# Kernel optimization log

Measured on AMD Instinct MI355X. Metric: run time of the kernel, lower is better.

## Reference

```python
import jax, jax.numpy as jnp
import numpy as np

HEADS = 4
DIM_HEAD = 32
SCALE = 16.0
EPS = 1e-5  # jax.nn.standardize default


def _standardize(t):
    # standardize over last axis (the flattened x*y*z sequence), per (b, h, d)
    mu = jnp.mean(t, axis=-1, keepdims=True)
    var = jnp.var(t, axis=-1, keepdims=True)
    return (t - mu) * jax.lax.rsqrt(var + EPS)


def setup_inputs() -> dict:
    key = jax.random.key(0)
    k1, k2, k3 = jax.random.split(key, 3)
    dim = 64
    hidden = HEADS * DIM_HEAD  # 128
    b, x, y, z = 2, 16, 16, 16
    inp = jax.random.normal(k1, (b, x, y, z, dim), dtype=jnp.float32)
    # 1x1x1 convs == pointwise channel matmuls; init like flax lecun_normal-ish scale
    w_qkv = jax.random.normal(k2, (dim, 3 * hidden), dtype=jnp.float32) / np.sqrt(dim)
    w_out = jax.random.normal(k3, (hidden, dim), dtype=jnp.float32) / np.sqrt(hidden)
    b_out = jnp.zeros((dim,), dtype=jnp.float32)
    return {"input": inp, "w_qkv": w_qkv, "w_out": w_out, "b_out": b_out}


def reference(input, w_qkv, w_out, b_out):
    b, x, y, z, c = input.shape
    s = x * y * z
    # pointwise conv -> qkv
    qkv = jnp.einsum('bxyzc,cd->bxyzd', input, w_qkv)  # [b,x,y,z,3*hidden]
    q, k, v = jnp.split(qkv, 3, axis=-1)
    # rearrange 'b x y z (h c) -> b h c (x y z)'
    def to_bhds(t):
        return t.reshape(b, s, HEADS, DIM_HEAD).transpose(0, 2, 3, 1)  # [b,h,d,s]
    q, k, v = map(to_bhds, (q, k, v))
    q = _standardize(q)
    k = _standardize(k)
    sim = jnp.einsum('bhdi,bhdj->bhij', q, k) * SCALE  # [b,h,s,s]
    attn = jax.nn.softmax(sim, axis=-1)
    out = jnp.einsum('bhij,bhdj->bhid', attn, v)  # [b,h,s,d]
    # rearrange 'b h (x y z) d -> b x y z (h d)'
    out = out.transpose(0, 2, 1, 3).reshape(b, x, y, z, HEADS * DIM_HEAD)
    return jnp.einsum('bxyzc,co->bxyzo', out, w_out) + b_out
```

## Files before the change

### kernel.cpp

```cpp
#include <hip/hip_runtime.h>
#include <math.h>
#include <stdint.h>


typedef __attribute__((ext_vector_type(8))) short short8;
typedef __attribute__((ext_vector_type(4))) float f32x4;
typedef __attribute__((ext_vector_type(16))) float f32x16;

#define QSCALE 23.083120654223414f

#if __has_builtin(__builtin_amdgcn_exp2f)
#define EXP2F(x) __builtin_amdgcn_exp2f(x)
#else
#define EXP2F(x) exp2f(x)
#endif

__device__ inline uint32_t pack_hilo(float y) {
  uint32_t uy = __float_as_uint(y);
  uint32_t hb = (uy + 0x7fffu + ((uy >> 16) & 1u)) >> 16;
  float hf = __uint_as_float(hb << 16);
  float r = y - hf;
  uint32_t ur = __float_as_uint(r);
  uint32_t lb = (ur + 0x7fffu + ((ur >> 16) & 1u)) >> 16;
  return (hb << 16) | (lb & 0xffffu);
}

__device__ inline ushort f32_to_bf16(float y) {
  uint32_t uy = __float_as_uint(y);
  return (ushort)((uy + 0x7fffu + ((uy >> 16) & 1u)) >> 16);
}

__device__ inline float bpermf(int addr, float v) {
  return __int_as_float(__builtin_amdgcn_ds_bpermute(addr, __float_as_int(v)));
}

__device__ inline short8 as_s8(uint4 v) {
  union { uint4 u; short8 s; } t;
  t.u = v;
  return t.s;
}

__global__ __launch_bounds__(256) void qkv_kernel(const float* __restrict__ in,
                                                  const float* __restrict__ w,
                                                  float* __restrict__ qf,
                                                  float* __restrict__ kf,
                                                  ushort* __restrict__ vfr,
                                                  float* __restrict__ psum,
                                                  float* __restrict__ psq) {
  __shared__ char smem[18432];
  __shared__ float ssum[64], ssq[64];
  ushort* Bh = (ushort*)smem;
  ushort* Bl = (ushort*)(smem + 9216);
  float* VT = (float*)smem;

  const int ctile = blockIdx.x % 6;
  const int stile = blockIdx.x / 6;
  const int tid = threadIdx.x;
  const int row0 = stile * 64;
  const int sel = ctile >> 1;

  if (tid < 64) { ssum[tid] = 0.f; ssq[tid] = 0.f; }

  {
    const int col = tid & 63;
    const int k0 = (tid >> 6) * 16;
    const float* wp = w + (size_t)k0 * 384 + ctile * 64 + col;
    float xv[16];
#pragma unroll
    for (int j = 0; j < 16; ++j) xv[j] = wp[(size_t)j * 384];
    uint32_t hi[8], lo[8];
#pragma unroll
    for (int p = 0; p < 8; ++p) {
      const uint32_t u0 = __float_as_uint(xv[2 * p]);
      const uint32_t u1 = __float_as_uint(xv[2 * p + 1]);
      hi[p] = __builtin_amdgcn_perm(u1, u0, 0x07060302u);
      const float d0 = xv[2 * p] - __uint_as_float(u0 & 0xffff0000u);
      const float d1 = xv[2 * p + 1] - __uint_as_float(u1 & 0xffff0000u);
      lo[p] = __builtin_amdgcn_perm(__float_as_uint(d1), __float_as_uint(d0), 0x07060302u);
    }
    uint4* bh = (uint4*)&Bh[col * 72 + k0];
    bh[0] = make_uint4(hi[0], hi[1], hi[2], hi[3]);
    bh[1] = make_uint4(hi[4], hi[5], hi[6], hi[7]);
    uint4* bl = (uint4*)&Bl[col * 72 + k0];
    bl[0] = make_uint4(lo[0], lo[1], lo[2], lo[3]);
    bl[1] = make_uint4(lo[4], lo[5], lo[6], lo[7]);
  }
  __syncthreads();

  const int wv = tid >> 6, lane = tid & 63;
  const int wr = wv >> 1, wc = wv & 1;
  const int h2 = lane >> 5, pl = lane & 31;

  short8 ah[4], al[4];
  {
    const float* ap = in + (size_t)(row0 + wr * 32 + pl) * 64 + h2 * 8;
#pragma unroll
    for (int kb = 0; kb < 4; ++kb) {
      const float4 xa = *(const float4*)(ap + kb * 16);
      const float4 xb = *(const float4*)(ap + kb * 16 + 4);
      const float xs[8] = {xa.x, xa.y, xa.z, xa.w, xb.x, xb.y, xb.z, xb.w};
      uint32_t hp[4], lp[4];
#pragma unroll
      for (int p = 0; p < 4; ++p) {
        const uint32_t u0 = __float_as_uint(xs[2 * p]);
        const uint32_t u1 = __float_as_uint(xs[2 * p + 1]);
        hp[p] = __builtin_amdgcn_perm(u1, u0, 0x07060302u);
        const float d0 = xs[2 * p] - __uint_as_float(u0 & 0xffff0000u);
        const float d1 = xs[2 * p + 1] - __uint_as_float(u1 & 0xffff0000u);
        lp[p] = __builtin_amdgcn_perm(__float_as_uint(d1), __float_as_uint(d0), 0x07060302u);
      }
      union { uint32_t u[4]; short8 s; } th, tl;
      th.u[0] = hp[0]; th.u[1] = hp[1]; th.u[2] = hp[2]; th.u[3] = hp[3];
      tl.u[0] = lp[0]; tl.u[1] = lp[1]; tl.u[2] = lp[2]; tl.u[3] = lp[3];
      ah[kb] = th.s;
      al[kb] = tl.s;
    }
  }

  const ushort* bhp = &Bh[(wc * 32 + pl) * 72 + h2 * 8];
  const ushort* blp = &Bl[(wc * 32 + pl) * 72 + h2 * 8];
  f32x16 acc = {};
#pragma unroll
  for (int kb = 0; kb < 4; ++kb) {
    const short8 bh = *(const short8*)(bhp + kb * 16);
    const short8 bl = *(const short8*)(blp + kb * 16);
    acc = __builtin_amdgcn_mfma_f32_32x32x16_bf16(ah[kb], bh, acc, 0, 0, 0);
    acc = __builtin_amdgcn_mfma_f32_32x32x16_bf16(ah[kb], bl, acc, 0, 0, 0);
    acc = __builtin_amdgcn_mfma_f32_32x32x16_bf16(al[kb], bh, acc, 0, 0, 0);
  }

  const int b = row0 >> 12;
  const int sl0 = (row0 & 4095) + wr * 32;
  const int chg = ctile * 64 + wc * 32 + pl;

  if (sel < 2) {
    const int hd0 = chg & 127;
    const int h = hd0 >> 5, d0 = hd0 & 31;
    float* dst = (sel == 0 ? qf : kf) + ((size_t)(b * 4 + h) * 4096 + sl0) * 32 + d0;
    float s1 = 0.f, s2 = 0.f;
#pragma unroll
    for (int reg = 0; reg < 16; ++reg) {
      const int r = (reg & 3) + 8 * (reg >> 2) + 4 * h2;
      dst[(size_t)r * 32] = acc[reg];
      s1 += acc[reg];
      s2 += acc[reg] * acc[reg];
    }
    atomicAdd(&ssum[wc * 32 + pl], s1);
    atomicAdd(&ssq[wc * 32 + pl], s2);
    __syncthreads();
    if (tid < 64) {
      const int ch = (ctile & 1) * 64 + tid;
      const int idx = (((sel * 2 + b) * 128) + ch) * 64 + (stile & 63);
      psum[idx] = ssum[tid];
      psq[idx] = ssq[tid];
    }
  } else {
    __syncthreads();
    const int chv = wc * 32 + pl;
#pragma unroll
    for (int reg = 0; reg < 16; ++reg) {
      const int r = wr * 32 + (reg & 3) + 8 * (reg >> 2) + 4 * h2;
      VT[chv * 68 + r] = acc[reg];
    }
    __syncthreads();
    const int jt0 = (row0 & 4095) >> 5;
#pragma unroll
    for (int hl = 0; hl < 2; ++hl) {
      const int jtl = tid >> 7, c = (tid >> 6) & 1, ln = tid & 63;
      const int d = ln & 31, hh = ln >> 5;
      const int jloc = 32 * jtl + 16 * c + 8 * hh;
      const int ch = hl * 32 + d;
      const float4 f0 = *(const float4*)&VT[ch * 68 + jloc];
      const float4 f1 = *(const float4*)&VT[ch * 68 + jloc + 4];
      uint4 pk;
      pk.x = (uint32_t)f32_to_bf16(f0.x) | ((uint32_t)f32_to_bf16(f0.y) << 16);
      pk.y = (uint32_t)f32_to_bf16(f0.z) | ((uint32_t)f32_to_bf16(f0.w) << 16);
      pk.z = (uint32_t)f32_to_bf16(f1.x) | ((uint32_t)f32_to_bf16(f1.y) << 16);
      pk.w = (uint32_t)f32_to_bf16(f1.z) | ((uint32_t)f32_to_bf16(f1.w) << 16);
      const int h = (ctile - 4) * 2 + hl;
      ushort* dst =
          vfr + (((size_t)((b * 4 + h) * 128 + jt0 + jtl) * 2 + c) * 64 + ln) * 8;
      *(uint4*)dst = pk;
    }
  }
}

__global__ __launch_bounds__(256) void norm_kernel(const float* __restrict__ qf,
                                                   const float* __restrict__ kf,
                                                   ushort* __restrict__ qfr_hi,
                                                   ushort* __restrict__ qfr_lo,
                                                   ushort* __restrict__ kfr_hi,
                                                   ushort* __restrict__ kfr_lo,
                                                   const float* __restrict__ psum,
                                                   const float* __restrict__ psq) {
  const int bx = blockIdx.x;
  const int tensor = bx >> 7;
  const int bh = (bx >> 4) & 7;
  const int s0 = (bx & 15) * 256;
  const int tid = threadIdx.x;
  __shared__ float red[2][32][8];
  __shared__ float tA[32], tB[32];
  {
    const int d = tid >> 3, p = tid & 7;
    const int base = ((tensor * 2 + (bh >> 2)) * 128 + (bh & 3) * 32 + d) * 64 + p * 8;
    float sm = 0.f, sq = 0.f;
#pragma unroll
    for (int e = 0; e < 8; ++e) {
      sm += psum[base + e];
      sq += psq[base + e];
    }
    red[0][d][p] = sm;
    red[1][d][p] = sq;
  }
  __syncthreads();
  if (tid < 32) {
    float sm = 0.f, sq = 0.f;
#pragma unroll
    for (int e = 0; e < 8; ++e) {
      sm += red[0][tid][e];
      sq += red[1][tid][e];
    }
    const float mu = sm * (1.f / 4096.f);
    const float scale = tensor == 0 ? QSCALE : 1.0f;
    const float inv = rsqrtf(sq * (1.f / 4096.f) - mu * mu + 1e-5f) * scale;
    tA[tid] = inv;
    tB[tid] = -mu * inv;
  }
  __syncthreads();

  const float* src = (tensor == 0 ? qf : kf) + (size_t)bh * 4096 * 32;
  ushort* dhi = (tensor == 0 ? qfr_hi : kfr_hi) + (size_t)(bh * 128 + (s0 >> 5)) * 1024;
  ushort* dlo = (tensor == 0 ? qfr_lo : kfr_lo) + (size_t)(bh * 128 + (s0 >> 5)) * 1024;
#pragma unroll
  for (int pass = 0; pass < 4; ++pass) {
    const int idx = tid + pass * 256;
    const int jtl = idx >> 7;
    const int c = (idx >> 6) & 1;
    const int ln = idx & 63;
    const int p = ln & 31, hh = ln >> 5;
    const int row = tensor == 0 ? p : ((p & 0x13) | ((p & 4) << 1) | ((p & 8) >> 1));
    const int s = s0 + 32 * jtl + row;
    const int d0 = 16 * c + 8 * hh;
    const float4 x0 = *(const float4*)&src[(size_t)s * 32 + d0];
    const float4 x1 = *(const float4*)&src[(size_t)s * 32 + d0 + 4];
    const float4 A0 = *(const float4*)&tA[d0];
    const float4 A1 = *(const float4*)&tA[d0 + 4];
    const float4 B0 = *(const float4*)&tB[d0];
    const float4 B1 = *(const float4*)&tB[d0 + 4];
    uint32_t pk[8];
    pk[0] = pack_hilo(fmaf(x0.x, A0.x, B0.x));
    pk[1] = pack_hilo(fmaf(x0.y, A0.y, B0.y));
    pk[2] = pack_hilo(fmaf(x0.z, A0.z, B0.z));
    pk[3] = pack_hilo(fmaf(x0.w, A0.w, B0.w));
    pk[4] = pack_hilo(fmaf(x1.x, A1.x, B1.x));
    pk[5] = pack_hilo(fmaf(x1.y, A1.y, B1.y));
    pk[6] = pack_hilo(fmaf(x1.z, A1.z, B1.z));
    pk[7] = pack_hilo(fmaf(x1.w, A1.w, B1.w));
    uint4 HV, LV;
    HV.x = __builtin_amdgcn_perm(pk[1], pk[0], 0x07060302u);
    HV.y = __builtin_amdgcn_perm(pk[3], pk[2], 0x07060302u);
    HV.z = __builtin_amdgcn_perm(pk[5], pk[4], 0x07060302u);
    HV.w = __builtin_amdgcn_perm(pk[7], pk[6], 0x07060302u);
    LV.x = __builtin_amdgcn_perm(pk[1], pk[0], 0x05040100u);
    LV.y = __builtin_amdgcn_perm(pk[3], pk[2], 0x05040100u);
    LV.z = __builtin_amdgcn_perm(pk[5], pk[4], 0x05040100u);
    LV.w = __builtin_amdgcn_perm(pk[7], pk[6], 0x05040100u);
    const size_t doff = ((size_t)(jtl * 2 + c) * 64 + ln) * 8;
    *(uint4*)(dhi + doff) = HV;
    *(uint4*)(dlo + doff) = LV;
  }
}

__global__ __launch_bounds__(512, 4) void attn_kernel(const ushort* __restrict__ qfr_hi,
                                                      const ushort* __restrict__ qfr_lo,
                                                      const ushort* __restrict__ kfr_hi,
                                                      const ushort* __restrict__ kfr_lo,
                                                      const ushort* __restrict__ vfr,
                                                      float* __restrict__ o) {
  __shared__ float OM[8 * 32 * 36];
  __shared__ float ML[8 * 64];

  const int tid = threadIdx.x;
  const int w = tid >> 6;
  const int js = w;
  const int lane = tid & 63;
  const int pl = lane & 31, h2 = lane >> 5;
  const int bh = blockIdx.x & 7;
  const int it = blockIdx.x >> 3;

  const size_t qbase = (size_t)(bh * 128 + it) * 1024 + lane * 8;
  const short8 qh0 = *(const short8*)(qfr_hi + qbase);
  const short8 qh1 = *(const short8*)(qfr_hi + qbase + 512);
  const short8 ql0 = *(const short8*)(qfr_lo + qbase);
  const short8 ql1 = *(const short8*)(qfr_lo + qbase + 512);

  const int bp32 = (lane ^ 32) << 2;

  const size_t kbase = (size_t)(bh * 128 + js * 16) * 1024 + lane * 8;
  const ushort* kh = kfr_hi + kbase;
  const ushort* kl = kfr_lo + kbase;
  const ushort* vp = vfr + kbase;

  f32x16 oacc;
#pragma unroll
  for (int r = 0; r < 16; ++r) oacc[r] = 0.f;
  const f32x16 zf = {};
  float m = -INFINITY, l = 0.f;

  uint4 rk0 = *(const uint4*)(kh);
  uint4 rk1 = *(const uint4*)(kh + 512);
  uint4 rl0 = *(const uint4*)(kl);
  uint4 rl1 = *(const uint4*)(kl + 512);
  uint4 rv0 = *(const uint4*)(vp);
  uint4 rv1 = *(const uint4*)(vp + 512);

  for (int t = 0; t < 16; ++t) {
    const short8 ck0 = as_s8(rk0), ck1 = as_s8(rk1);
    const short8 cl0 = as_s8(rl0), cl1 = as_s8(rl1);
    const short8 cv0 = as_s8(rv0), cv1 = as_s8(rv1);
    {
      const int off = (t + 1) * 1024;
      rk0 = *(const uint4*)(kh + off);
      rk1 = *(const uint4*)(kh + off + 512);
      rl0 = *(const uint4*)(kl + off);
      rl1 = *(const uint4*)(kl + off + 512);
      rv0 = *(const uint4*)(vp + off);
      rv1 = *(const uint4*)(vp + off + 512);
    }

    __builtin_amdgcn_s_setprio(1);
    f32x16 sc = __builtin_amdgcn_mfma_f32_32x32x16_bf16(ck0, qh0, zf, 0, 0, 0);
    sc = __builtin_amdgcn_mfma_f32_32x32x16_bf16(ck1, qh1, sc, 0, 0, 0);
    sc = __builtin_amdgcn_mfma_f32_32x32x16_bf16(ck0, ql0, sc, 0, 0, 0);
    sc = __builtin_amdgcn_mfma_f32_32x32x16_bf16(ck1, ql1, sc, 0, 0, 0);
    sc = __builtin_amdgcn_mfma_f32_32x32x16_bf16(cl0, qh0, sc, 0, 0, 0);
    sc = __builtin_amdgcn_mfma_f32_32x32x16_bf16(cl1, qh1, sc, 0, 0, 0);
    __builtin_amdgcn_s_setprio(0);

    const float x0 = fmaxf(fmaxf(sc[0], sc[1]), sc[2]);
    const float x1 = fmaxf(fmaxf(sc[3], sc[4]), sc[5]);
    const float x2 = fmaxf(fmaxf(sc[6], sc[7]), sc[8]);
    const float x3 = fmaxf(fmaxf(sc[9], sc[10]), sc[11]);
    const float x4 = fmaxf(fmaxf(sc[12], sc[13]), sc[14]);
    float mx = fmaxf(fmaxf(fmaxf(x0, x1), x2), fmaxf(fmaxf(x3, x4), sc[15]));
    mx = fmaxf(mx, bpermf(bp32, mx));
    const float mn = fmaxf(m, mx);
    const float al = EXP2F(m - mn);
    m = mn;
#pragma unroll
    for (int r = 0; r < 16; ++r) sc[r] = EXP2F(sc[r] - mn);
    const float s0 = sc[0] + sc[1], s1 = sc[2] + sc[3];
    const float s2 = sc[4] + sc[5], s3 = sc[6] + sc[7];
    const float s4 = sc[8] + sc[9], s5 = sc[10] + sc[11];
    const float s6 = sc[12] + sc[13], s7 = sc[14] + sc[15];
    float rs = ((s0 + s1) + (s2 + s3)) + ((s4 + s5) + (s6 + s7));
    rs += bpermf(bp32, rs);
    l = l * al + rs;
#pragma unroll
    for (int r = 0; r < 16; ++r) oacc[r] *= al;

    uint32_t pk[8];
#pragma unroll
    for (int i = 0; i < 8; ++i)
      pk[i] = __builtin_amdgcn_perm(__float_as_uint(sc[2 * i + 1]),
                                    __float_as_uint(sc[2 * i]), 0x07060302u);
    union { uint32_t u4[4]; short8 s8; } p0, p1;
    p0.u4[0] = pk[0]; p0.u4[1] = pk[1]; p0.u4[2] = pk[2]; p0.u4[3] = pk[3];
    p1.u4[0] = pk[4]; p1.u4[1] = pk[5]; p1.u4[2] = pk[6]; p1.u4[3] = pk[7];

    __builtin_amdgcn_s_setprio(1);
    oacc = __builtin_amdgcn_mfma_f32_32x32x16_bf16(cv0, p0.s8, oacc, 0, 0, 0);
    oacc = __builtin_amdgcn_mfma_f32_32x32x16_bf16(cv1, p1.s8, oacc, 0, 0, 0);
    __builtin_amdgcn_s_setprio(0);
  }

  {
    float* om = OM + (size_t)(w * 32 + pl) * 36;
#pragma unroll
    for (int g = 0; g < 4; ++g)
      *(float4*)&om[4 * h2 + 8 * g] =
          make_float4(oacc[4 * g], oacc[4 * g + 1], oacc[4 * g + 2], oacc[4 * g + 3]);
    if (h2 == 0) {
      ML[w * 64 + pl] = m;
      ML[w * 64 + 32 + pl] = l;
    }
  }
  __syncthreads();
  const int b = bh >> 2, h = bh & 3;
#pragma unroll
  for (int pass = 0; pass < 2; ++pass) {
    const int idx = tid + pass * 512;
    const int i = idx >> 5;
    const int d = idx & 31;
    float mk[8], lk[8];
#pragma unroll
    for (int k = 0; k < 8; ++k) {
      mk[k] = ML[k * 64 + i];
      lk[k] = ML[k * 64 + 32 + i];
    }
    const float M01 = fmaxf(mk[0], mk[1]), M23 = fmaxf(mk[2], mk[3]);
    const float M45 = fmaxf(mk[4], mk[5]), M67 = fmaxf(mk[6], mk[7]);
    const float M = fmaxf(fmaxf(M01, M23), fmaxf(M45, M67));
    float L = 0.f, V = 0.f;
#pragma unroll
    for (int k = 0; k < 8; ++k) {
      const float wk = EXP2F(mk[k] - M);
      L += lk[k] * wk;
      V += OM[(k * 32 + i) * 36 + d] * wk;
    }
    const float val = V * (1.001953125f / L);
    const int ig = it * 32 + i;
    o[((size_t)(b * 4096) + ig) * 128 + h * 32 + d] = val;
  }
}

__global__ __launch_bounds__(256) void proj_kernel(const float* __restrict__ o,
                                                   const float* __restrict__ w,
                                                   const float* __restrict__ bias,
                                                   float* __restrict__ out) {
  __shared__ float wT[64 * 132];
  const int tid = threadIdx.x;
  for (int idx = tid; idx < 8192; idx += 256) {
    const int c = idx >> 6, col = idx & 63;
    const int g = (c >> 2) ^ ((col >> 3) & 7);
    wT[col * 132 + (g << 2) + (c & 3)] = w[idx];
  }
  __syncthreads();
  const int col = tid & 63;
  const int r = blockIdx.x * 8 + ((tid >> 6) << 1);
  const float* r0 = o + (size_t)r * 128;
  const float* r1 = r0 + 128;
  const int wbase = col * 132;
  const int gx = (col >> 3) & 7;
  float a0 = bias[col], a1 = a0;
  for (int c = 0; c < 128; c += 4) {
    const float4 x0 = *(const float4*)&r0[c];
    const float4 x1 = *(const float4*)&r1[c];
    const float4 wv = *(const float4*)&wT[wbase + ((((c >> 2) ^ gx)) << 2)];
    a0 = fmaf(x0.x, wv.x, a0); a0 = fmaf(x0.y, wv.y, a0);
    a0 = fmaf(x0.z, wv.z, a0); a0 = fmaf(x0.w, wv.w, a0);
    a1 = fmaf(x1.x, wv.x, a1); a1 = fmaf(x1.y, wv.y, a1);
    a1 = fmaf(x1.z, wv.z, a1); a1 = fmaf(x1.w, wv.w, a1);
  }
  out[(size_t)r * 64 + col] = a0;
  out[(size_t)(r + 1) * 64 + col] = a1;
}

extern "C" void kernel_launch(void* const* d_in, const int* in_sizes, int n_in,
                              void* d_out, int out_size, void* d_ws, size_t ws_size,
                              hipStream_t stream) {
  const float* input = (const float*)d_in[0];
  const float* w_qkv = (const float*)d_in[1];
  const float* w_out = (const float*)d_in[2];
  const float* b_out = (const float*)d_in[3];

  char* W = (char*)d_ws;
  float* qf = (float*)(W + 0);
  float* kf = (float*)(W + (4u << 20));
  ushort* kfr_hi = (ushort*)(W + (8u << 20));
  ushort* kfr_lo = (ushort*)(W + (10u << 20));
  ushort* vfr = (ushort*)(W + (12u << 20));
  ushort* qfr_hi = (ushort*)(W + (14u << 20));
  ushort* qfr_lo = (ushort*)(W + (16u << 20));
  float* psum = (float*)(W + (18u << 20));
  float* psq = (float*)(W + (18u << 20) + (128u << 10));
  float* ob = qf;
  float* out = (float*)d_out;

  hipLaunchKernelGGL(qkv_kernel, dim3(768), dim3(256), 0, stream, input, w_qkv, qf, kf,
                     vfr, psum, psq);
  hipLaunchKernelGGL(norm_kernel, dim3(256), dim3(256), 0, stream, qf, kf, qfr_hi,
                     qfr_lo, kfr_hi, kfr_lo, psum, psq);
  hipLaunchKernelGGL(attn_kernel, dim3(1024), dim3(512), 0, stream, qfr_hi, qfr_lo,
                     kfr_hi, kfr_lo, vfr, ob);
  hipLaunchKernelGGL(proj_kernel, dim3(1024), dim3(256), 0, stream, ob, w_out, b_out, out);
}
```

Measured before the change: 131.6 us.

## Fuse output projection into attention kernel with atomic accumulation

Removes the separate projection kernel. Each attention block now multiplies its per-head output tile by the matching 32x64 slice of w_out and atomically adds the result into the final output, which the qkv kernel pre-fills with the bias. The softmax subtract, sum and rescale steps are also rewritten on two-wide float vectors so they can map to packed FP32 instructions. This saves one launch and the round trip of the intermediate attention output through memory, but adds four-way atomic contention per output element, a summation order that is no longer deterministic, and extra shared-memory work at the end of each attention block.

```diff
diff --git a/kernel.cpp b/kernel.cpp
--- a/kernel.cpp
+++ b/kernel.cpp
@@ -4,6 +4,7 @@
 
 
 typedef __attribute__((ext_vector_type(8))) short short8;
+typedef __attribute__((ext_vector_type(2))) float f32x2;
 typedef __attribute__((ext_vector_type(4))) float f32x4;
 typedef __attribute__((ext_vector_type(16))) float f32x16;
 
@@ -46,7 +47,9 @@
                                                   float* __restrict__ kf,
                                                   ushort* __restrict__ vfr,
                                                   float* __restrict__ psum,
-                                                  float* __restrict__ psq) {
+                                                  float* __restrict__ psq,
+                                                  const float* __restrict__ bias,
+                                                  float* __restrict__ out) {
   __shared__ char smem[18432];
   __shared__ float ssum[64], ssq[64];
   ushort* Bh = (ushort*)smem;
@@ -58,6 +61,9 @@
   const int tid = threadIdx.x;
   const int row0 = stile * 64;
   const int sel = ctile >> 1;
+
+  for (int i = blockIdx.x * 256 + tid; i < 8192 * 64; i += 768 * 256)
+    out[i] = bias[i & 63];
 
   if (tid < 64) { ssum[tid] = 0.f; ssq[tid] = 0.f; }
 
@@ -276,7 +282,8 @@
                                                       const ushort* __restrict__ kfr_hi,
                                                       const ushort* __restrict__ kfr_lo,
                                                       const ushort* __restrict__ vfr,
-                                                      float* __restrict__ o) {
+                                                      const float* __restrict__ wout,
+                                                      float* __restrict__ out) {
   __shared__ float OM[8 * 32 * 36];
   __shared__ float ML[8 * 64];
 
@@ -301,9 +308,9 @@
   const ushort* kl = kfr_lo + kbase;
   const ushort* vp = vfr + kbase;
 
-  f32x16 oacc;
-#pragma unroll
-  for (int r = 0; r < 16; ++r) oacc[r] = 0.f;
+  union { f32x16 v; f32x2 p[8]; } oac;
+#pragma unroll
+  for (int r = 0; r < 16; ++r) oac.v[r] = 0.f;
   const f32x16 zf = {};
   float m = -INFINITY, l = 0.f;
 
@@ -329,48 +336,53 @@
     }
 
     __builtin_amdgcn_s_setprio(1);
-    f32x16 sc = __builtin_amdgcn_mfma_f32_32x32x16_bf16(ck0, qh0, zf, 0, 0, 0);
-    sc = __builtin_amdgcn_mfma_f32_32x32x16_bf16(ck1, qh1, sc, 0, 0, 0);
-    sc = __builtin_amdgcn_mfma_f32_32x32x16_bf16(ck0, ql0, sc, 0, 0, 0);
-    sc = __builtin_amdgcn_mfma_f32_32x32x16_bf16(ck1, ql1, sc, 0, 0, 0);
-    sc = __builtin_amdgcn_mfma_f32_32x32x16_bf16(cl0, qh0, sc, 0, 0, 0);
-    sc = __builtin_amdgcn_mfma_f32_32x32x16_bf16(cl1, qh1, sc, 0, 0, 0);
+    union { f32x16 v; f32x2 p[8]; } sc;
+    sc.v = __builtin_amdgcn_mfma_f32_32x32x16_bf16(ck0, qh0, zf, 0, 0, 0);
+    sc.v = __builtin_amdgcn_mfma_f32_32x32x16_bf16(ck1, qh1, sc.v, 0, 0, 0);
+    sc.v = __builtin_amdgcn_mfma_f32_32x32x16_bf16(ck0, ql0, sc.v, 0, 0, 0);
+    sc.v = __builtin_amdgcn_mfma_f32_32x32x16_bf16(ck1, ql1, sc.v, 0, 0, 0);
+    sc.v = __builtin_amdgcn_mfma_f32_32x32x16_bf16(cl0, qh0, sc.v, 0, 0, 0);
+    sc.v = __builtin_amdgcn_mfma_f32_32x32x16_bf16(cl1, qh1, sc.v, 0, 0, 0);
     __builtin_amdgcn_s_setprio(0);
 
-    const float x0 = fmaxf(fmaxf(sc[0], sc[1]), sc[2]);
-    const float x1 = fmaxf(fmaxf(sc[3], sc[4]), sc[5]);
-    const float x2 = fmaxf(fmaxf(sc[6], sc[7]), sc[8]);
-    const float x3 = fmaxf(fmaxf(sc[9], sc[10]), sc[11]);
-    const float x4 = fmaxf(fmaxf(sc[12], sc[13]), sc[14]);
-    float mx = fmaxf(fmaxf(fmaxf(x0, x1), x2), fmaxf(fmaxf(x3, x4), sc[15]));
+    const float x0 = fmaxf(fmaxf(sc.v[0], sc.v[1]), sc.v[2]);
+    const float x1 = fmaxf(fmaxf(sc.v[3], sc.v[4]), sc.v[5]);
+    const float x2 = fmaxf(fmaxf(sc.v[6], sc.v[7]), sc.v[8]);
+    const float x3 = fmaxf(fmaxf(sc.v[9], sc.v[10]), sc.v[11]);
+    const float x4 = fmaxf(fmaxf(sc.v[12], sc.v[13]), sc.v[14]);
+    float mx = fmaxf(fmaxf(fmaxf(x0, x1), x2), fmaxf(fmaxf(x3, x4), sc.v[15]));
     mx = fmaxf(mx, bpermf(bp32, mx));
     const float mn = fmaxf(m, mx);
     const float al = EXP2F(m - mn);
     m = mn;
-#pragma unroll
-    for (int r = 0; r < 16; ++r) sc[r] = EXP2F(sc[r] - mn);
-    const float s0 = sc[0] + sc[1], s1 = sc[2] + sc[3];
-    const float s2 = sc[4] + sc[5], s3 = sc[6] + sc[7];
-    const float s4 = sc[8] + sc[9], s5 = sc[10] + sc[11];
-    const float s6 = sc[12] + sc[13], s7 = sc[14] + sc[15];
-    float rs = ((s0 + s1) + (s2 + s3)) + ((s4 + s5) + (s6 + s7));
+    const f32x2 mn2 = {mn, mn};
+#pragma unroll
+    for (int i = 0; i < 8; ++i) sc.p[i] = sc.p[i] - mn2;
+#pragma unroll
+    for (int r = 0; r < 16; ++r) sc.v[r] = EXP2F(sc.v[r]);
+    const f32x2 a0 = sc.p[0] + sc.p[1], a1 = sc.p[2] + sc.p[3];
+    const f32x2 a2 = sc.p[4] + sc.p[5], a3 = sc.p[6] + sc.p[7];
+    const f32x2 b0 = a0 + a1, b1 = a2 + a3;
+    const f32x2 c0 = b0 + b1;
+    float rs = c0.x + c0.y;
     rs += bpermf(bp32, rs);
     l = l * al + rs;
-#pragma unroll
-    for (int r = 0; r < 16; ++r) oacc[r] *= al;
+    const f32x2 al2 = {al, al};
+#pragma unroll
+    for (int i = 0; i < 8; ++i) oac.p[i] = oac.p[i] * al2;
 
     uint32_t pk[8];
 #pragma unroll
     for (int i = 0; i < 8; ++i)
-      pk[i] = __builtin_amdgcn_perm(__float_as_uint(sc[2 * i + 1]),
-                                    __float_as_uint(sc[2 * i]), 0x07060302u);
+      pk[i] = __builtin_amdgcn_perm(__float_as_uint(sc.v[2 * i + 1]),
+                                    __float_as_uint(sc.v[2 * i]), 0x07060302u);
     union { uint32_t u4[4]; short8 s8; } p0, p1;
     p0.u4[0] = pk[0]; p0.u4[1] = pk[1]; p0.u4[2] = pk[2]; p0.u4[3] = pk[3];
     p1.u4[0] = pk[4]; p1.u4[1] = pk[5]; p1.u4[2] = pk[6]; p1.u4[3] = pk[7];
 
     __builtin_amdgcn_s_setprio(1);
-    oacc = __builtin_amdgcn_mfma_f32_32x32x16_bf16(cv0, p0.s8, oacc, 0, 0, 0);
-    oacc = __builtin_amdgcn_mfma_f32_32x32x16_bf16(cv1, p1.s8, oacc, 0, 0, 0);
+    oac.v = __builtin_amdgcn_mfma_f32_32x32x16_bf16(cv0, p0.s8, oac.v, 0, 0, 0);
+    oac.v = __builtin_amdgcn_mfma_f32_32x32x16_bf16(cv1, p1.s8, oac.v, 0, 0, 0);
     __builtin_amdgcn_s_setprio(0);
   }
 
@@ -379,7 +391,7 @@
 #pragma unroll
     for (int g = 0; g < 4; ++g)
       *(float4*)&om[4 * h2 + 8 * g] =
-          make_float4(oacc[4 * g], oacc[4 * g + 1], oacc[4 * g + 2], oacc[4 * g + 3]);
+          make_float4(oac.v[4 * g], oac.v[4 * g + 1], oac.v[4 * g + 2], oac.v[4 * g + 3]);
     if (h2 == 0) {
       ML[w * 64 + pl] = m;
       ML[w * 64 + 32 + pl] = l;
@@ -387,6 +399,7 @@
   }
   __syncthreads();
   const int b = bh >> 2, h = bh & 3;
+  float vals[2];
 #pragma unroll
   for (int pass = 0; pass < 2; ++pass) {
     const int idx = tid + pass * 512;
@@ -408,42 +421,29 @@
       L += lk[k] * wk;
       V += OM[(k * 32 + i) * 36 + d] * wk;
     }
-    const float val = V * (1.001953125f / L);
-    const int ig = it * 32 + i;
-    o[((size_t)(b * 4096) + ig) * 128 + h * 32 + d] = val;
-  }
-}
-
-__global__ __launch_bounds__(256) void proj_kernel(const float* __restrict__ o,
-                                                   const float* __restrict__ w,
-                                                   const float* __restrict__ bias,
-                                                   float* __restrict__ out) {
-  __shared__ float wT[64 * 132];
-  const int tid = threadIdx.x;
-  for (int idx = tid; idx < 8192; idx += 256) {
-    const int c = idx >> 6, col = idx & 63;
-    const int g = (c >> 2) ^ ((col >> 3) & 7);
-    wT[col * 132 + (g << 2) + (c & 3)] = w[idx];
-  }
-  __syncthreads();
-  const int col = tid & 63;
-  const int r = blockIdx.x * 8 + ((tid >> 6) << 1);
-  const float* r0 = o + (size_t)r * 128;
-  const float* r1 = r0 + 128;
-  const int wbase = col * 132;
-  const int gx = (col >> 3) & 7;
-  float a0 = bias[col], a1 = a0;
-  for (int c = 0; c < 128; c += 4) {
-    const float4 x0 = *(const float4*)&r0[c];
-    const float4 x1 = *(const float4*)&r1[c];
-    const float4 wv = *(const float4*)&wT[wbase + ((((c >> 2) ^ gx)) << 2)];
-    a0 = fmaf(x0.x, wv.x, a0); a0 = fmaf(x0.y, wv.y, a0);
-    a0 = fmaf(x0.z, wv.z, a0); a0 = fmaf(x0.w, wv.w, a0);
-    a1 = fmaf(x1.x, wv.x, a1); a1 = fmaf(x1.y, wv.y, a1);
-    a1 = fmaf(x1.z, wv.z, a1); a1 = fmaf(x1.w, wv.w, a1);
-  }
-  out[(size_t)r * 64 + col] = a0;
-  out[(size_t)(r + 1) * 64 + col] = a1;
+    vals[pass] = V * (1.001953125f / L);
+  }
+  __syncthreads();
+
+  float* V2 = OM;
+  float* WL = OM + 1024;
+#pragma unroll
+  for (int pass = 0; pass < 2; ++pass) V2[tid + pass * 512] = vals[pass];
+  {
+    const float* wsrc = wout + (size_t)h * 32 * 64;
+#pragma unroll
+    for (int p = 0; p < 4; ++p) WL[tid + p * 512] = wsrc[tid + p * 512];
+  }
+  __syncthreads();
+#pragma unroll
+  for (int p = 0; p < 4; ++p) {
+    const int idx = tid + p * 512;
+    const int i = idx >> 6, col = idx & 63;
+    float acc = 0.f;
+#pragma unroll
+    for (int d = 0; d < 32; ++d) acc = fmaf(V2[i * 32 + d], WL[d * 64 + col], acc);
+    atomicAdd(&out[((size_t)(b * 4096) + it * 32 + i) * 64 + col], acc);
+  }
 }
 
 extern "C" void kernel_launch(void* const* d_in, const int* in_sizes, int n_in,
@@ -464,14 +464,12 @@
   ushort* qfr_lo = (ushort*)(W + (16u << 20));
   float* psum = (float*)(W + (18u << 20));
   float* psq = (float*)(W + (18u << 20) + (128u << 10));
-  float* ob = qf;
   float* out = (float*)d_out;
 
   hipLaunchKernelGGL(qkv_kernel, dim3(768), dim3(256), 0, stream, input, w_qkv, qf, kf,
-                     vfr, psum, psq);
+                     vfr, psum, psq, b_out, out);
   hipLaunchKernelGGL(norm_kernel, dim3(256), dim3(256), 0, stream, qf, kf, qfr_hi,
                      qfr_lo, kfr_hi, kfr_lo, psum, psq);
   hipLaunchKernelGGL(attn_kernel, dim3(1024), dim3(512), 0, stream, qfr_hi, qfr_lo,
-                     kfr_hi, kfr_lo, vfr, ob);
-  hipLaunchKernelGGL(proj_kernel, dim3(1024), dim3(256), 0, stream, ob, w_out, b_out, out);
-}
+                     kfr_hi, kfr_lo, vfr, w_out, out);
+}
```

New measurement: 125.5 us. 1.05x faster.
